# Kernel optimization log

Hardware: AMD Instinct MI355X
Metric: run time of the kernel (lower is better)

The kernel has to match this reference:

```python
import jax, jax.numpy as jnp
import numpy as np

B, H, T, D = 2, 8, 2048, 64
STATE = H * D  # 512

def setup_inputs() -> dict:
    key = jax.random.key(0)
    kq, kk, kv, kw, kl = jax.random.split(key, 5)
    q = jax.random.normal(kq, (B * H, T, D), jnp.float32)
    k = jax.random.normal(kk, (B * H, T, D), jnp.float32)
    v = jax.random.normal(kv, (B * H, T, D), jnp.float32)
    # causal position mask: True = masked (future positions)
    position_mask = jnp.triu(jnp.ones((T, T), dtype=bool), 1)
    # per-batch source lengths in [T//2, T]; True = padding (masked)
    lengths = jax.random.randint(kl, (B,), T // 2, T + 1)
    src_length_mask = jnp.arange(T)[None, :] >= lengths[:, None]
    W_merge = jax.random.normal(kw, (STATE, STATE), jnp.float32) / np.sqrt(STATE)
    return {"q": q, "k": k, "v": v, "position_mask": position_mask,
            "src_length_mask": src_length_mask, "W_merge": W_merge}

def reference(q, k, v, position_mask, src_length_mask, W_merge):
    bb, n_dest, d = q.shape              # bb = B*H
    n_batch = src_length_mask.shape[0]
    n_heads = bb // n_batch
    scale = 1.0 / np.sqrt(d)
    # [bb, T_dest, T_src] full score matrix (as in the torch bmm)
    logits = jnp.einsum('btd,bsd->bts', q, k) * scale
    logits = logits.reshape(n_batch, n_heads, n_dest, -1)
    logits = jnp.where(position_mask[None, None], -jnp.inf, logits)
    logits = jnp.where(src_length_mask[:, None, None, :], -jnp.inf, logits)
    scores = jax.nn.softmax(logits, axis=-1).reshape(bb, n_dest, -1)
    # dropout p=0 (eval) -> identity
    out = jnp.einsum('bts,bsd->btd', scores, v)
    out = out.reshape(n_batch, n_heads, n_dest, d).transpose(0, 2, 1, 3)
    out = out.reshape(n_batch, n_dest, n_heads * d)
    return out @ W_merge.T  # bias-free Linear merge
```

## Files before the change

kernel.cpp:

```cpp
#include <hip/hip_runtime.h>

#define TT 2048
#define DD 64
#define NSTATE 512

typedef __attribute__((ext_vector_type(8))) short short8;
typedef __attribute__((ext_vector_type(4))) short short4v;
typedef __attribute__((ext_vector_type(4))) float f4;

union U8 { short8 s; unsigned u[4]; };
union U4 { short4v s; unsigned u[2]; };

__device__ __forceinline__ unsigned pk_bf16(float lo, float hi) {
  unsigned r;
  asm("v_cvt_pk_bf16_f32 %0, %1, %2" : "=v"(r) : "v"(lo), "v"(hi));
  return r;
}
__device__ __forceinline__ unsigned short f2bf1(float x) {
  return (unsigned short)(pk_bf16(x, x) & 0xFFFFu);
}

__device__ __forceinline__ bool mask_at(const void* p, bool u8, int idx) {
  return u8 ? (((const unsigned char*)p)[idx] != 0)
            : (((const int*)p)[idx] != 0);
}

__device__ __forceinline__ void gld16(const void* g, void* l) {
  __builtin_amdgcn_global_load_lds(
      (const __attribute__((address_space(1))) void*)g,
      (__attribute__((address_space(3))) void*)l, 16, 0, 0);
}

__global__ __launch_bounds__(256)
void prep_kernel(const float* __restrict__ k, const float* __restrict__ v,
                 const float* __restrict__ W, const void* __restrict__ posmask,
                 const void* __restrict__ srcmask,
                 unsigned short* __restrict__ Wb, unsigned short* __restrict__ Kimg,
                 unsigned short* __restrict__ VTimg, int* __restrict__ lenbuf) {
  const int bidx = blockIdx.x;
  const int tid = threadIdx.x;
  if (bidx < 512) {
    const int bh = bidx >> 5, tile = bidx & 31;
    const float* kp = k + (bh * TT + tile * 64) * DD;
    unsigned short* dst = Kimg + (bh * 32 + tile) * 4096;
#pragma unroll
    for (int t2 = 0; t2 < 2; ++t2) {
      int j = tid + t2 * 256;
      int c8 = j >> 6, r6 = j & 63;
      int kb = c8 >> 1, cc = c8 & 1, qd = r6 >> 4, klo = r6 & 15;
      int key = kb * 16 + klo, dg = cc * 4 + qd;
      f4 a0 = *(const f4*)(kp + key * DD + dg * 8);
      f4 a1 = *(const f4*)(kp + key * DD + dg * 8 + 4);
      U8 o;
      o.u[0] = pk_bf16(a0[0], a0[1]); o.u[1] = pk_bf16(a0[2], a0[3]);
      o.u[2] = pk_bf16(a1[0], a1[1]); o.u[3] = pk_bf16(a1[2], a1[3]);
      *(short8*)(dst + j * 8) = o.s;
    }
    __shared__ float Vt[64][65];
    const float* vp = v + (bh * TT + tile * 64) * DD;
    {
      int key = tid >> 2, c0 = (tid & 3) * 16;
#pragma unroll
      for (int i = 0; i < 4; ++i) {
        f4 x = *(const f4*)(vp + key * DD + c0 + i * 4);
        Vt[key][c0 + i * 4 + 0] = x[0];
        Vt[key][c0 + i * 4 + 1] = x[1];
        Vt[key][c0 + i * 4 + 2] = x[2];
        Vt[key][c0 + i * 4 + 3] = x[3];
      }
    }
    __syncthreads();
    unsigned short* vd = VTimg + (bh * 32 + tile) * 4096;
#pragma unroll
    for (int t2 = 0; t2 < 2; ++t2) {
      int j = tid + t2 * 256;
      int fs = j >> 5;
      int db = fs >> 2, sb = fs & 3;
      int jj = j & 31;
      float t[8];
#pragma unroll
      for (int ii = 0; ii < 8; ++ii) {
        int l = jj * 2 + (ii >> 2), r = ii & 3;
        int s = sb * 16 + (l >> 4) * 4 + r;
        int d = db * 16 + (l & 15);
        t[ii] = Vt[s][d];
      }
      U8 o;
      o.u[0] = pk_bf16(t[0], t[1]); o.u[1] = pk_bf16(t[2], t[3]);
      o.u[2] = pk_bf16(t[4], t[5]); o.u[3] = pk_bf16(t[6], t[7]);
      *(short8*)(vd + j * 8) = o.s;
    }
  } else if (bidx < 768) {
    int i = ((bidx - 512) * 256 + tid) * 4;
    f4 x = *(const f4*)(W + i);
    U4 o;
    o.u[0] = pk_bf16(x[0], x[1]); o.u[1] = pk_bf16(x[2], x[3]);
    *(short4v*)(Wb + i) = o.s;
  } else {
    const int wv = tid >> 6, lane = tid & 63;
    if (wv < 2) {
      const bool u8 = (((const unsigned char*)posmask)[1] != 0);
      int pos = 1024 + lane * 16;
      bool m1 = mask_at(srcmask, u8, wv * TT + pos);
      unsigned long long bal = __ballot(m1);
      int cur = bal ? (1024 + (__ffsll((unsigned long long)bal) - 1) * 16) : 2048;
      int prev = cur - 16;
      bool m2 = false;
      if (lane < 16) {
        int pos2 = prev + 1 + lane;
        m2 = (pos2 < TT) ? mask_at(srcmask, u8, wv * TT + pos2) : true;
      }
      unsigned long long bal2 = __ballot(m2);
      int len = prev + 1 + (__ffsll((unsigned long long)bal2) - 1);
      if (lane == 0) lenbuf[wv] = len;
    }
  }
}

__global__ __launch_bounds__(512, 4)
void attn_kernel(const float* __restrict__ q, const unsigned short* __restrict__ Kimg,
                 const unsigned short* __restrict__ VTimg,
                 const int* __restrict__ lenbuf, unsigned short* __restrict__ merged) {
  const int i = blockIdx.x;
  const int bh = ((i & 7) << 1) | ((i >> 3) & 1);
  const int tr = i >> 4;
  const int tile = (tr < 16) ? tr : 47 - tr;
  const int b = bh >> 3, h = bh & 7;
  const int tid = threadIdx.x;
  const int w = tid >> 6, lane = tid & 63;
  const int g = w >> 2, wl = w & 3;
  const int lane_lo = lane & 15, quad = lane >> 4;
  const int q0 = tile * 64 + wl * 16;
  const int len = lenbuf[b];
  const int n_st = min(tile + 1, (len + 63) >> 6);
  const int trips = (n_st + 1) >> 1;

  __shared__ __attribute__((aligned(16))) unsigned short Klds[2][2][4096];
  __shared__ __attribute__((aligned(16))) unsigned short Vlds[2][2][4096];

  short8 qf[2];
  {
    const float* qrow = q + ((bh * TT) + q0 + lane_lo) * DD;
#pragma unroll
    for (int c = 0; c < 2; ++c) {
      int d0 = c * 32 + quad * 8;
      f4 a0 = *(const f4*)(qrow + d0);
      f4 a1 = *(const f4*)(qrow + d0 + 4);
      U8 t;
      t.u[0] = pk_bf16(a0[0] * 0.125f, a0[1] * 0.125f);
      t.u[1] = pk_bf16(a0[2] * 0.125f, a0[3] * 0.125f);
      t.u[2] = pk_bf16(a1[0] * 0.125f, a1[1] * 0.125f);
      t.u[3] = pk_bf16(a1[2] * 0.125f, a1[3] * 0.125f);
      qf[c] = t.s;
    }
  }
  asm volatile("s_waitcnt vmcnt(0)" ::: "memory");

  float l_lane = 0.f;
  f4 O[4];
#pragma unroll
  for (int d = 0; d < 4; ++d) O[d] = (f4){0.f, 0.f, 0.f, 0.f};

  const char* kbase = (const char*)Kimg + (size_t)bh * 262144;
  const char* vbase = (const char*)VTimg + (size_t)bh * 262144;

  auto stage = [&](int st, int bufi) {
    const char* ks = kbase + st * 8192 + wl * 2048 + lane * 16;
    char* kl = (char*)&Klds[g][bufi][0] + wl * 2048 + lane * 16;
    gld16(ks, kl); gld16(ks + 1024, kl + 1024);
    const char* vs = vbase + st * 8192 + wl * 2048 + lane * 16;
    char* vl = (char*)&Vlds[g][bufi][0] + wl * 2048 + lane * 16;
    gld16(vs, vl); gld16(vs + 1024, vl + 1024);
  };

  if (g < n_st) stage(g, 0);

  for (int it = 0; it < trips; ++it) {
    const int st = 2 * it + g;
    const int bufc = it & 1;
    if (st + 2 < n_st) {
      stage(st + 2, bufc ^ 1);
      asm volatile("s_waitcnt vmcnt(4)" ::: "memory");
    } else {
      asm volatile("s_waitcnt vmcnt(0)" ::: "memory");
    }
    __builtin_amdgcn_s_barrier();
    __builtin_amdgcn_sched_barrier(0);

    if (st < n_st) {
      const unsigned short* Kl = &Klds[g][bufc][0];
      const unsigned short* Vl = &Vlds[g][bufc][0];
      const int s0 = st * 64;

      f4 ST[4];
      __builtin_amdgcn_s_setprio(1);
#pragma unroll
      for (int sb = 0; sb < 4; ++sb) {
        f4 acc = (f4){0.f, 0.f, 0.f, 0.f};
#pragma unroll
        for (int c = 0; c < 2; ++c) {
          short8 kf = *(const short8*)&Kl[((sb * 2 + c) * 64 + lane) * 8];
          acc = __builtin_amdgcn_mfma_f32_16x16x32_bf16(kf, qf[c], acc, 0, 0, 0);
        }
        ST[sb] = acc;
      }
      __builtin_amdgcn_s_setprio(0);

      const bool edge = (st == tile) || (s0 + 64 > len);
      const int tq = q0 + lane_lo;
      short4v pf[4];
#pragma unroll
      for (int sb = 0; sb < 4; ++sb) {
        float e[4];
#pragma unroll
        for (int r = 0; r < 4; ++r) {
          float p = __expf(ST[sb][r]);
          if (edge) {
            int s = s0 + sb * 16 + quad * 4 + r;
            if (s > tq || s >= len) p = 0.f;
          }
          l_lane += p;
          e[r] = p;
        }
        U4 pu;
        pu.u[0] = pk_bf16(e[0], e[1]);
        pu.u[1] = pk_bf16(e[2], e[3]);
        pf[sb] = pu.s;
      }

      __builtin_amdgcn_s_setprio(1);
#pragma unroll
      for (int db = 0; db < 4; ++db) {
        f4 acc = O[db];
#pragma unroll
        for (int sb = 0; sb < 4; ++sb) {
          short4v vf = *(const short4v*)&Vl[(db * 4 + sb) * 256 + lane * 4];
          acc = __builtin_amdgcn_mfma_f32_16x16x16bf16_1k(pf[sb], vf, acc, 0, 0, 0);
        }
        O[db] = acc;
      }
      __builtin_amdgcn_s_setprio(0);
    }
    __builtin_amdgcn_sched_barrier(0);
    __builtin_amdgcn_s_barrier();
  }

  l_lane += __shfl_xor(l_lane, 16);
  l_lane += __shfl_xor(l_lane, 32);

  float* Ored = (float*)&Klds[1][0][0];
  float* lred = (float*)&Vlds[1][0][0];
  if (g == 1) {
    float* po = Ored + (wl * 64 + lane) * 16;
#pragma unroll
    for (int db = 0; db < 4; ++db) *(f4*)(po + db * 4) = O[db];
    lred[wl * 64 + lane] = l_lane;
  }
  __syncthreads();
  if (g == 0) {
    const float* po = Ored + (wl * 64 + lane) * 16;
#pragma unroll
    for (int db = 0; db < 4; ++db) {
      f4 o1 = *(const f4*)(po + db * 4);
      O[db][0] += o1[0]; O[db][1] += o1[1];
      O[db][2] += o1[2]; O[db][3] += o1[3];
    }
    l_lane += lred[wl * 64 + lane];
    float inv = 1.0f / l_lane;
    float invr[4];
#pragma unroll
    for (int r = 0; r < 4; ++r) invr[r] = __shfl(inv, quad * 4 + r);
#pragma unroll
    for (int db = 0; db < 4; ++db)
#pragma unroll
      for (int r = 0; r < 4; ++r) {
        int t = q0 + quad * 4 + r;
        merged[((b * TT) + t) * NSTATE + h * DD + db * 16 + lane_lo] =
            f2bf1(O[db][r] * invr[r]);
      }
  }
}

__global__ __launch_bounds__(512)
void merge_kernel(const unsigned short* __restrict__ A,
                  const unsigned short* __restrict__ Wb,
                  float* __restrict__ out) {
  __shared__ __attribute__((aligned(16))) unsigned short Wl[64 * 512];
  const int tid = threadIdx.x;
  const int n0 = blockIdx.x * 64, m0 = blockIdx.y * 128;
  {
    int row = tid >> 3, cb = (tid & 7) * 8;
    const unsigned short* src = Wb + (n0 + row) * NSTATE;
#pragma unroll
    for (int j = 0; j < 8; ++j) {
      int c = cb + j;
      int phys = c ^ (row & 7);
      *(short8*)&Wl[row * 512 + phys * 8] = *(const short8*)(src + c * 8);
    }
  }
  __syncthreads();

  const int w = tid >> 6, lane = tid & 63;
  const int lo16 = lane & 15, quad = lane >> 4;
  const int m = m0 + w * 16;
  f4 acc[4];
#pragma unroll
  for (int nf = 0; nf < 4; ++nf) acc[nf] = (f4){0.f, 0.f, 0.f, 0.f};
  const unsigned short* arow = A + (m + lo16) * NSTATE + quad * 8;
#pragma unroll 4
  for (int k0 = 0; k0 < NSTATE; k0 += 32) {
    short8 af = *(const short8*)(arow + k0);
#pragma unroll
    for (int nf = 0; nf < 4; ++nf) {
      int n = nf * 16 + lo16;
      int phys = ((k0 >> 3) + quad) ^ (n & 7);
      short8 bf = *(const short8*)&Wl[n * 512 + phys * 8];
      acc[nf] = __builtin_amdgcn_mfma_f32_16x16x32_bf16(af, bf, acc[nf], 0, 0, 0);
    }
  }
#pragma unroll
  for (int nf = 0; nf < 4; ++nf)
#pragma unroll
    for (int r = 0; r < 4; ++r)
      out[(m + quad * 4 + r) * NSTATE + n0 + nf * 16 + lo16] = acc[nf][r];
}

extern "C" void kernel_launch(void* const* d_in, const int* in_sizes, int n_in,
                              void* d_out, int out_size, void* d_ws, size_t ws_size,
                              hipStream_t stream) {
  (void)in_sizes; (void)n_in; (void)out_size; (void)ws_size;
  const float* q = (const float*)d_in[0];
  const float* k = (const float*)d_in[1];
  const float* v = (const float*)d_in[2];
  const void* posm = d_in[3];
  const void* srcm = d_in[4];
  const float* W = (const float*)d_in[5];
  float* out = (float*)d_out;

  unsigned short* merged = (unsigned short*)d_ws;
  unsigned short* Wb     = merged + 2097152;
  unsigned short* Kimg   = Wb + 262144;
  unsigned short* VTimg  = Kimg + 2097152;
  int* lenbuf = (int*)(VTimg + 2097152);

  prep_kernel<<<dim3(769), dim3(256), 0, stream>>>(k, v, W, posm, srcm,
                                                   Wb, Kimg, VTimg, lenbuf);
  attn_kernel<<<dim3(512), dim3(512), 0, stream>>>(q, Kimg, VTimg, lenbuf, merged);
  merge_kernel<<<dim3(8, 32), dim3(512), 0, stream>>>(merged, Wb, out);
}
```

Before: 121.1 us.

## Split attention keys four ways with 32-row query tiles per warp

Each warp now handles 32 query rows, up from 16, so every K and V fragment read from LDS feeds two MFMAs. The key dimension is split into 32-key sub-tiles across four warp groups instead of 64-key tiles across two, and the V image layout is rearranged so one 16-byte load supplies both halves. Sub-tiles that lie entirely above a warp's causal diagonal are skipped. In exchange the cross-group reduction of O and l through shared memory grows from one partner group to three, and register pressure rises.

```diff
diff --git a/kernel.cpp b/kernel.cpp
--- a/kernel.cpp
+++ b/kernel.cpp
@@ -18,6 +18,13 @@
 }
 __device__ __forceinline__ unsigned short f2bf1(float x) {
   return (unsigned short)(pk_bf16(x, x) & 0xFFFFu);
+}
+
+__device__ __forceinline__ short4v lo4(short8 x) {
+  short4v r; r[0] = x[0]; r[1] = x[1]; r[2] = x[2]; r[3] = x[3]; return r;
+}
+__device__ __forceinline__ short4v hi4(short8 x) {
+  short4v r; r[0] = x[4]; r[1] = x[5]; r[2] = x[6]; r[3] = x[7]; return r;
 }
 
 __device__ __forceinline__ bool mask_at(const void* p, bool u8, int idx) {
@@ -74,14 +81,14 @@
 #pragma unroll
     for (int t2 = 0; t2 < 2; ++t2) {
       int j = tid + t2 * 256;
-      int fs = j >> 5;
-      int db = fs >> 2, sb = fs & 3;
-      int jj = j & 31;
+      int hd = j >> 6;
+      int hh = hd >> 2, db = hd & 3;
+      int l = j & 63;
       float t[8];
 #pragma unroll
       for (int ii = 0; ii < 8; ++ii) {
-        int l = jj * 2 + (ii >> 2), r = ii & 3;
-        int s = sb * 16 + (l >> 4) * 4 + r;
+        int sbl = ii >> 2, r = ii & 3;
+        int s = hh * 32 + sbl * 16 + (l >> 4) * 4 + r;
         int d = db * 16 + (l & 15);
         t[ii] = Vt[s][d];
       }
@@ -128,19 +135,19 @@
   const int b = bh >> 3, h = bh & 7;
   const int tid = threadIdx.x;
   const int w = tid >> 6, lane = tid & 63;
-  const int g = w >> 2, wl = w & 3;
+  const int g = w >> 1, wl = w & 1;
   const int lane_lo = lane & 15, quad = lane >> 4;
-  const int q0 = tile * 64 + wl * 16;
+  const int q0 = tile * 64 + wl * 32;
   const int len = lenbuf[b];
-  const int n_st = min(tile + 1, (len + 63) >> 6);
-  const int trips = (n_st + 1) >> 1;
-
-  __shared__ __attribute__((aligned(16))) unsigned short Klds[2][2][4096];
-  __shared__ __attribute__((aligned(16))) unsigned short Vlds[2][2][4096];
-
-  short8 qf[2];
-  {
-    const float* qrow = q + ((bh * TT) + q0 + lane_lo) * DD;
+  const int n_ss = min(2 * (tile + 1), (len + 31) >> 5);
+  const int trips = (n_ss + 3) >> 2;
+
+  __shared__ __attribute__((aligned(16))) unsigned char smem[65536];
+
+  short8 qf[2][2];
+#pragma unroll
+  for (int qb = 0; qb < 2; ++qb) {
+    const float* qrow = q + ((bh * TT) + q0 + qb * 16 + lane_lo) * DD;
 #pragma unroll
     for (int c = 0; c < 2; ++c) {
       int d0 = c * 32 + quad * 8;
@@ -151,35 +158,38 @@
       t.u[1] = pk_bf16(a0[2] * 0.125f, a0[3] * 0.125f);
       t.u[2] = pk_bf16(a1[0] * 0.125f, a1[1] * 0.125f);
       t.u[3] = pk_bf16(a1[2] * 0.125f, a1[3] * 0.125f);
-      qf[c] = t.s;
+      qf[qb][c] = t.s;
     }
   }
   asm volatile("s_waitcnt vmcnt(0)" ::: "memory");
 
-  float l_lane = 0.f;
-  f4 O[4];
-#pragma unroll
-  for (int d = 0; d < 4; ++d) O[d] = (f4){0.f, 0.f, 0.f, 0.f};
+  float l_lane[2] = {0.f, 0.f};
+  f4 O[2][4];
+#pragma unroll
+  for (int qb = 0; qb < 2; ++qb)
+#pragma unroll
+    for (int d = 0; d < 4; ++d) O[qb][d] = (f4){0.f, 0.f, 0.f, 0.f};
 
   const char* kbase = (const char*)Kimg + (size_t)bh * 262144;
   const char* vbase = (const char*)VTimg + (size_t)bh * 262144;
 
-  auto stage = [&](int st, int bufi) {
-    const char* ks = kbase + st * 8192 + wl * 2048 + lane * 16;
-    char* kl = (char*)&Klds[g][bufi][0] + wl * 2048 + lane * 16;
-    gld16(ks, kl); gld16(ks + 1024, kl + 1024);
-    const char* vs = vbase + st * 8192 + wl * 2048 + lane * 16;
-    char* vl = (char*)&Vlds[g][bufi][0] + wl * 2048 + lane * 16;
-    gld16(vs, vl); gld16(vs + 1024, vl + 1024);
+  auto stage = [&](int ss, int bufi) {
+    const int gl = wl * 64 + lane;
+    const char* ks = kbase + ss * 4096 + gl * 16;
+    char* kl = (char*)smem + (g * 2 + bufi) * 4096 + gl * 16;
+    gld16(ks, kl); gld16(ks + 2048, kl + 2048);
+    const char* vs = vbase + ss * 4096 + gl * 16;
+    char* vl = (char*)smem + 32768 + (g * 2 + bufi) * 4096 + gl * 16;
+    gld16(vs, vl); gld16(vs + 2048, vl + 2048);
   };
 
-  if (g < n_st) stage(g, 0);
+  if (g < n_ss) stage(g, 0);
 
   for (int it = 0; it < trips; ++it) {
-    const int st = 2 * it + g;
+    const int ss = 4 * it + g;
     const int bufc = it & 1;
-    if (st + 2 < n_st) {
-      stage(st + 2, bufc ^ 1);
+    if (ss + 4 < n_ss) {
+      stage(ss + 4, bufc ^ 1);
       asm volatile("s_waitcnt vmcnt(4)" ::: "memory");
     } else {
       asm volatile("s_waitcnt vmcnt(0)" ::: "memory");
@@ -187,57 +197,61 @@
     __builtin_amdgcn_s_barrier();
     __builtin_amdgcn_sched_barrier(0);
 
-    if (st < n_st) {
-      const unsigned short* Kl = &Klds[g][bufc][0];
-      const unsigned short* Vl = &Vlds[g][bufc][0];
-      const int s0 = st * 64;
-
-      f4 ST[4];
+    const int s0 = ss * 32;
+    if (ss < n_ss && s0 <= q0 + 31) {
+      const unsigned short* Kl = (const unsigned short*)smem + (g * 2 + bufc) * 2048;
+      const unsigned short* Vl = (const unsigned short*)smem + 16384 + (g * 2 + bufc) * 2048;
+
+      f4 ST[2][2];
       __builtin_amdgcn_s_setprio(1);
 #pragma unroll
-      for (int sb = 0; sb < 4; ++sb) {
-        f4 acc = (f4){0.f, 0.f, 0.f, 0.f};
+      for (int sbl = 0; sbl < 2; ++sbl) {
+        f4 a0 = (f4){0.f, 0.f, 0.f, 0.f};
+        f4 a1 = (f4){0.f, 0.f, 0.f, 0.f};
 #pragma unroll
         for (int c = 0; c < 2; ++c) {
-          short8 kf = *(const short8*)&Kl[((sb * 2 + c) * 64 + lane) * 8];
-          acc = __builtin_amdgcn_mfma_f32_16x16x32_bf16(kf, qf[c], acc, 0, 0, 0);
+          short8 kf = *(const short8*)&Kl[((sbl * 2 + c) * 64 + lane) * 8];
+          a0 = __builtin_amdgcn_mfma_f32_16x16x32_bf16(kf, qf[0][c], a0, 0, 0, 0);
+          a1 = __builtin_amdgcn_mfma_f32_16x16x32_bf16(kf, qf[1][c], a1, 0, 0, 0);
         }
-        ST[sb] = acc;
+        ST[0][sbl] = a0; ST[1][sbl] = a1;
       }
       __builtin_amdgcn_s_setprio(0);
 
-      const bool edge = (st == tile) || (s0 + 64 > len);
-      const int tq = q0 + lane_lo;
-      short4v pf[4];
-#pragma unroll
-      for (int sb = 0; sb < 4; ++sb) {
-        float e[4];
-#pragma unroll
-        for (int r = 0; r < 4; ++r) {
-          float p = __expf(ST[sb][r]);
-          if (edge) {
-            int s = s0 + sb * 16 + quad * 4 + r;
-            if (s > tq || s >= len) p = 0.f;
+      const bool edge = (ss >= 2 * tile) || (s0 + 32 > len);
+      short4v pf[2][2];
+#pragma unroll
+      for (int qb = 0; qb < 2; ++qb) {
+        const int tq = q0 + qb * 16 + lane_lo;
+#pragma unroll
+        for (int sbl = 0; sbl < 2; ++sbl) {
+          float e[4];
+#pragma unroll
+          for (int r = 0; r < 4; ++r) {
+            float p = __expf(ST[qb][sbl][r]);
+            if (edge) {
+              int s = s0 + sbl * 16 + quad * 4 + r;
+              if (s > tq || s >= len) p = 0.f;
+            }
+            l_lane[qb] += p;
+            e[r] = p;
           }
-          l_lane += p;
-          e[r] = p;
+          U4 pu;
+          pu.u[0] = pk_bf16(e[0], e[1]);
+          pu.u[1] = pk_bf16(e[2], e[3]);
+          pf[qb][sbl] = pu.s;
         }
-        U4 pu;
-        pu.u[0] = pk_bf16(e[0], e[1]);
-        pu.u[1] = pk_bf16(e[2], e[3]);
-        pf[sb] = pu.s;
       }
 
       __builtin_amdgcn_s_setprio(1);
 #pragma unroll
       for (int db = 0; db < 4; ++db) {
-        f4 acc = O[db];
-#pragma unroll
-        for (int sb = 0; sb < 4; ++sb) {
-          short4v vf = *(const short4v*)&Vl[(db * 4 + sb) * 256 + lane * 4];
-          acc = __builtin_amdgcn_mfma_f32_16x16x16bf16_1k(pf[sb], vf, acc, 0, 0, 0);
-        }
-        O[db] = acc;
+        short8 vv = *(const short8*)&Vl[(db * 64 + lane) * 8];
+        short4v v0 = lo4(vv), v1 = hi4(vv);
+        O[0][db] = __builtin_amdgcn_mfma_f32_16x16x16bf16_1k(pf[0][0], v0, O[0][db], 0, 0, 0);
+        O[0][db] = __builtin_amdgcn_mfma_f32_16x16x16bf16_1k(pf[0][1], v1, O[0][db], 0, 0, 0);
+        O[1][db] = __builtin_amdgcn_mfma_f32_16x16x16bf16_1k(pf[1][0], v0, O[1][db], 0, 0, 0);
+        O[1][db] = __builtin_amdgcn_mfma_f32_16x16x16bf16_1k(pf[1][1], v1, O[1][db], 0, 0, 0);
       }
       __builtin_amdgcn_s_setprio(0);
     }
@@ -245,39 +259,57 @@
     __builtin_amdgcn_s_barrier();
   }
 
-  l_lane += __shfl_xor(l_lane, 16);
-  l_lane += __shfl_xor(l_lane, 32);
-
-  float* Ored = (float*)&Klds[1][0][0];
-  float* lred = (float*)&Vlds[1][0][0];
-  if (g == 1) {
-    float* po = Ored + (wl * 64 + lane) * 16;
-#pragma unroll
-    for (int db = 0; db < 4; ++db) *(f4*)(po + db * 4) = O[db];
-    lred[wl * 64 + lane] = l_lane;
+#pragma unroll
+  for (int qb = 0; qb < 2; ++qb) {
+    l_lane[qb] += __shfl_xor(l_lane[qb], 16);
+    l_lane[qb] += __shfl_xor(l_lane[qb], 32);
+  }
+
+  float* Opub = (float*)smem;
+  float* lpub = (float*)(smem + 49152);
+  if (g > 0) {
+    const int slot = (g - 1) * 2 + wl;
+    float* po = Opub + slot * 2048 + lane * 32;
+#pragma unroll
+    for (int qb = 0; qb < 2; ++qb)
+#pragma unroll
+      for (int db = 0; db < 4; ++db)
+        *(f4*)(po + qb * 16 + db * 4) = O[qb][db];
+    lpub[slot * 128 + lane * 2 + 0] = l_lane[0];
+    lpub[slot * 128 + lane * 2 + 1] = l_lane[1];
   }
   __syncthreads();
   if (g == 0) {
-    const float* po = Ored + (wl * 64 + lane) * 16;
-#pragma unroll
-    for (int db = 0; db < 4; ++db) {
-      f4 o1 = *(const f4*)(po + db * 4);
-      O[db][0] += o1[0]; O[db][1] += o1[1];
-      O[db][2] += o1[2]; O[db][3] += o1[3];
-    }
-    l_lane += lred[wl * 64 + lane];
-    float inv = 1.0f / l_lane;
-    float invr[4];
-#pragma unroll
-    for (int r = 0; r < 4; ++r) invr[r] = __shfl(inv, quad * 4 + r);
-#pragma unroll
-    for (int db = 0; db < 4; ++db)
-#pragma unroll
-      for (int r = 0; r < 4; ++r) {
-        int t = q0 + quad * 4 + r;
-        merged[((b * TT) + t) * NSTATE + h * DD + db * 16 + lane_lo] =
-            f2bf1(O[db][r] * invr[r]);
-      }
+#pragma unroll
+    for (int sl = 0; sl < 3; ++sl) {
+      const int slot = sl * 2 + wl;
+      const float* po = Opub + slot * 2048 + lane * 32;
+#pragma unroll
+      for (int qb = 0; qb < 2; ++qb)
+#pragma unroll
+        for (int db = 0; db < 4; ++db) {
+          f4 o1 = *(const f4*)(po + qb * 16 + db * 4);
+          O[qb][db][0] += o1[0]; O[qb][db][1] += o1[1];
+          O[qb][db][2] += o1[2]; O[qb][db][3] += o1[3];
+        }
+      l_lane[0] += lpub[slot * 128 + lane * 2 + 0];
+      l_lane[1] += lpub[slot * 128 + lane * 2 + 1];
+    }
+#pragma unroll
+    for (int qb = 0; qb < 2; ++qb) {
+      float inv = 1.0f / l_lane[qb];
+      float invr[4];
+#pragma unroll
+      for (int r = 0; r < 4; ++r) invr[r] = __shfl(inv, quad * 4 + r);
+#pragma unroll
+      for (int db = 0; db < 4; ++db)
+#pragma unroll
+        for (int r = 0; r < 4; ++r) {
+          int t = q0 + qb * 16 + quad * 4 + r;
+          merged[((b * TT) + t) * NSTATE + h * DD + db * 16 + lane_lo] =
+              f2bf1(O[qb][db][r] * invr[r]);
+        }
+    }
   }
 }
 
```

New measurement: 123.3 us. Within noise of the previous version (+1.9%).

## Fuse merge projection into attention epilogue with atomic accumulation per head

Applied to the files above, without the earlier changes.

Removes the separate merge GEMM kernel and the bf16 intermediate buffer. Each attention block now stages its normalized 64x64 output tile in LDS, multiplies it by that head's 64-column slice of W_merge, and atomically adds the partial 64x512 products into the fp32 output. The prep kernel zeroes the output first. This saves one launch and a global round-trip of the merged activations, but adds eight-way float atomic traffic per output element, extra epilogue work in each attention block, and a summation order that is no longer deterministic.

```diff
diff --git a/kernel.cpp b/kernel.cpp
--- a/kernel.cpp
+++ b/kernel.cpp
@@ -36,9 +36,15 @@
                  const float* __restrict__ W, const void* __restrict__ posmask,
                  const void* __restrict__ srcmask,
                  unsigned short* __restrict__ Wb, unsigned short* __restrict__ Kimg,
-                 unsigned short* __restrict__ VTimg, int* __restrict__ lenbuf) {
+                 unsigned short* __restrict__ VTimg, int* __restrict__ lenbuf,
+                 float* __restrict__ out) {
   const int bidx = blockIdx.x;
   const int tid = threadIdx.x;
+  {
+    const f4 z = (f4){0.f, 0.f, 0.f, 0.f};
+    for (int j = bidx * 256 + tid; j < 524288; j += 769 * 256)
+      *(f4*)(out + j * 4) = z;
+  }
   if (bidx < 512) {
     const int bh = bidx >> 5, tile = bidx & 31;
     const float* kp = k + (bh * TT + tile * 64) * DD;
@@ -120,7 +126,8 @@
 __global__ __launch_bounds__(512, 4)
 void attn_kernel(const float* __restrict__ q, const unsigned short* __restrict__ Kimg,
                  const unsigned short* __restrict__ VTimg,
-                 const int* __restrict__ lenbuf, unsigned short* __restrict__ merged) {
+                 const int* __restrict__ lenbuf, const unsigned short* __restrict__ Wb,
+                 float* __restrict__ out) {
   const int i = blockIdx.x;
   const int bh = ((i & 7) << 1) | ((i >> 3) & 1);
   const int tr = i >> 4;
@@ -135,8 +142,7 @@
   const int n_st = min(tile + 1, (len + 63) >> 6);
   const int trips = (n_st + 1) >> 1;
 
-  __shared__ __attribute__((aligned(16))) unsigned short Klds[2][2][4096];
-  __shared__ __attribute__((aligned(16))) unsigned short Vlds[2][2][4096];
+  __shared__ __attribute__((aligned(16))) unsigned short smem[32768];
 
   short8 qf[2];
   {
@@ -166,10 +172,10 @@
 
   auto stage = [&](int st, int bufi) {
     const char* ks = kbase + st * 8192 + wl * 2048 + lane * 16;
-    char* kl = (char*)&Klds[g][bufi][0] + wl * 2048 + lane * 16;
+    char* kl = (char*)smem + (g * 2 + bufi) * 8192 + wl * 2048 + lane * 16;
     gld16(ks, kl); gld16(ks + 1024, kl + 1024);
     const char* vs = vbase + st * 8192 + wl * 2048 + lane * 16;
-    char* vl = (char*)&Vlds[g][bufi][0] + wl * 2048 + lane * 16;
+    char* vl = (char*)smem + 32768 + (g * 2 + bufi) * 8192 + wl * 2048 + lane * 16;
     gld16(vs, vl); gld16(vs + 1024, vl + 1024);
   };
 
@@ -188,8 +194,8 @@
     __builtin_amdgcn_sched_barrier(0);
 
     if (st < n_st) {
-      const unsigned short* Kl = &Klds[g][bufc][0];
-      const unsigned short* Vl = &Vlds[g][bufc][0];
+      const unsigned short* Kl = smem + (g * 2 + bufc) * 4096;
+      const unsigned short* Vl = smem + 16384 + (g * 2 + bufc) * 4096;
       const int s0 = st * 64;
 
       f4 ST[4];
@@ -248,8 +254,8 @@
   l_lane += __shfl_xor(l_lane, 16);
   l_lane += __shfl_xor(l_lane, 32);
 
-  float* Ored = (float*)&Klds[1][0][0];
-  float* lred = (float*)&Vlds[1][0][0];
+  float* Ored = (float*)((char*)smem + 16384);
+  float* lred = (float*)((char*)smem + 49152);
   if (g == 1) {
     float* po = Ored + (wl * 64 + lane) * 16;
 #pragma unroll
@@ -257,6 +263,8 @@
     lred[wl * 64 + lane] = l_lane;
   }
   __syncthreads();
+
+  unsigned short* Am = smem;
   if (g == 0) {
     const float* po = Ored + (wl * 64 + lane) * 16;
 #pragma unroll
@@ -274,55 +282,60 @@
     for (int db = 0; db < 4; ++db)
 #pragma unroll
       for (int r = 0; r < 4; ++r) {
-        int t = q0 + quad * 4 + r;
-        merged[((b * TT) + t) * NSTATE + h * DD + db * 16 + lane_lo] =
+        int m = wl * 16 + quad * 4 + r;
+        int d = db * 16 + lane_lo;
+        Am[m * 64 + (((d >> 3) ^ (m & 7)) * 8) + (d & 7)] =
             f2bf1(O[db][r] * invr[r]);
       }
   }
-}
-
-__global__ __launch_bounds__(512)
-void merge_kernel(const unsigned short* __restrict__ A,
-                  const unsigned short* __restrict__ Wb,
-                  float* __restrict__ out) {
-  __shared__ __attribute__((aligned(16))) unsigned short Wl[64 * 512];
-  const int tid = threadIdx.x;
-  const int n0 = blockIdx.x * 64, m0 = blockIdx.y * 128;
-  {
-    int row = tid >> 3, cb = (tid & 7) * 8;
-    const unsigned short* src = Wb + (n0 + row) * NSTATE;
-#pragma unroll
-    for (int j = 0; j < 8; ++j) {
-      int c = cb + j;
-      int phys = c ^ (row & 7);
-      *(short8*)&Wl[row * 512 + phys * 8] = *(const short8*)(src + c * 8);
-    }
-  }
   __syncthreads();
 
-  const int w = tid >> 6, lane = tid & 63;
-  const int lo16 = lane & 15, quad = lane >> 4;
-  const int m = m0 + w * 16;
-  f4 acc[4];
-#pragma unroll
-  for (int nf = 0; nf < 4; ++nf) acc[nf] = (f4){0.f, 0.f, 0.f, 0.f};
-  const unsigned short* arow = A + (m + lo16) * NSTATE + quad * 8;
-#pragma unroll 4
-  for (int k0 = 0; k0 < NSTATE; k0 += 32) {
-    short8 af = *(const short8*)(arow + k0);
-#pragma unroll
-    for (int nf = 0; nf < 4; ++nf) {
-      int n = nf * 16 + lo16;
-      int phys = ((k0 >> 3) + quad) ^ (n & 7);
-      short8 bf = *(const short8*)&Wl[n * 512 + phys * 8];
-      acc[nf] = __builtin_amdgcn_mfma_f32_16x16x32_bf16(af, bf, acc[nf], 0, 0, 0);
-    }
-  }
-#pragma unroll
-  for (int nf = 0; nf < 4; ++nf)
-#pragma unroll
-    for (int r = 0; r < 4; ++r)
-      out[(m + quad * 4 + r) * NSTATE + n0 + nf * 16 + lo16] = acc[nf][r];
+  short8 af[4][2];
+#pragma unroll
+  for (int mb = 0; mb < 4; ++mb)
+#pragma unroll
+    for (int c = 0; c < 2; ++c)
+      af[mb][c] = *(const short8*)&Am[(mb * 16 + lane_lo) * 64 +
+                                      (((c * 4 + quad) ^ (lane_lo & 7)) * 8)];
+  unsigned short* Wl = smem + 4096;
+  const unsigned short* wsrc = Wb + h * 64;
+  const int n0w = w * 32;
+#pragma unroll
+  for (int nh = 0; nh < 2; ++nh) {
+    {
+      int n = tid >> 1, cb = (tid & 1) * 4;
+      const unsigned short* src = wsrc + (nh * 256 + n) * NSTATE;
+#pragma unroll
+      for (int jj = 0; jj < 4; ++jj) {
+        int c8 = cb + jj;
+        *(short8*)&Wl[n * 64 + ((c8 ^ (n & 7)) * 8)] = *(const short8*)(src + c8 * 8);
+      }
+    }
+    __syncthreads();
+    short8 bfw[2][2];
+#pragma unroll
+    for (int nf = 0; nf < 2; ++nf)
+#pragma unroll
+      for (int c = 0; c < 2; ++c) {
+        int n = n0w + nf * 16 + lane_lo;
+        bfw[nf][c] = *(const short8*)&Wl[n * 64 + (((c * 4 + quad) ^ (n & 7)) * 8)];
+      }
+#pragma unroll
+    for (int mb = 0; mb < 4; ++mb)
+#pragma unroll
+      for (int nf = 0; nf < 2; ++nf) {
+        f4 acc = (f4){0.f, 0.f, 0.f, 0.f};
+        acc = __builtin_amdgcn_mfma_f32_16x16x32_bf16(af[mb][0], bfw[nf][0], acc, 0, 0, 0);
+        acc = __builtin_amdgcn_mfma_f32_16x16x32_bf16(af[mb][1], bfw[nf][1], acc, 0, 0, 0);
+#pragma unroll
+        for (int rr = 0; rr < 4; ++rr) {
+          int t = tile * 64 + mb * 16 + quad * 4 + rr;
+          atomicAdd(&out[((b * TT) + t) * NSTATE + nh * 256 + n0w + nf * 16 + lane_lo],
+                    acc[rr]);
+        }
+      }
+    if (nh == 0) __syncthreads();
+  }
 }
 
 extern "C" void kernel_launch(void* const* d_in, const int* in_sizes, int n_in,
@@ -337,14 +350,12 @@
   const float* W = (const float*)d_in[5];
   float* out = (float*)d_out;
 
-  unsigned short* merged = (unsigned short*)d_ws;
-  unsigned short* Wb     = merged + 2097152;
-  unsigned short* Kimg   = Wb + 262144;
-  unsigned short* VTimg  = Kimg + 2097152;
+  unsigned short* Wb   = (unsigned short*)d_ws;
+  unsigned short* Kimg = Wb + 262144;
+  unsigned short* VTimg = Kimg + 2097152;
   int* lenbuf = (int*)(VTimg + 2097152);
 
   prep_kernel<<<dim3(769), dim3(256), 0, stream>>>(k, v, W, posm, srcm,
-                                                   Wb, Kimg, VTimg, lenbuf);
-  attn_kernel<<<dim3(512), dim3(512), 0, stream>>>(q, Kimg, VTimg, lenbuf, merged);
-  merge_kernel<<<dim3(8, 32), dim3(512), 0, stream>>>(merged, Wb, out);
-}
+                                                   Wb, Kimg, VTimg, lenbuf, out);
+  attn_kernel<<<dim3(512), dim3(512), 0, stream>>>(q, Kimg, VTimg, lenbuf, Wb, out);
+}
```

Result: slower. 147.2 us (+21.5%).

## Halve attention tile to 32 queries and keys with 1024 smaller blocks

Applied to the files above, without the earlier changes.

The attention kernel now uses 256-thread blocks that each handle 32 query rows, stepping over 32-key sub-tiles. It launches 1024 blocks instead of 512, and the V image layout is reordered so one 16-byte LDS read feeds two MFMAs. The goal is better load balance across CUs for the causal triangle and less wasted work on diagonal and edge tiles, since the masking granularity becomes 32. The cost is more blocks, more barriers per key processed, and Q being reloaded more often relative to K/V traffic.

```diff
diff --git a/kernel.cpp b/kernel.cpp
--- a/kernel.cpp
+++ b/kernel.cpp
@@ -18,6 +18,13 @@
 }
 __device__ __forceinline__ unsigned short f2bf1(float x) {
   return (unsigned short)(pk_bf16(x, x) & 0xFFFFu);
+}
+
+__device__ __forceinline__ short4v lo4(short8 x) {
+  short4v r; r[0] = x[0]; r[1] = x[1]; r[2] = x[2]; r[3] = x[3]; return r;
+}
+__device__ __forceinline__ short4v hi4(short8 x) {
+  short4v r; r[0] = x[4]; r[1] = x[5]; r[2] = x[6]; r[3] = x[7]; return r;
 }
 
 __device__ __forceinline__ bool mask_at(const void* p, bool u8, int idx) {
@@ -74,14 +81,14 @@
 #pragma unroll
     for (int t2 = 0; t2 < 2; ++t2) {
       int j = tid + t2 * 256;
-      int fs = j >> 5;
-      int db = fs >> 2, sb = fs & 3;
-      int jj = j & 31;
+      int hd = j >> 6;
+      int hh = hd >> 2, db = hd & 3;
+      int l = j & 63;
       float t[8];
 #pragma unroll
       for (int ii = 0; ii < 8; ++ii) {
-        int l = jj * 2 + (ii >> 2), r = ii & 3;
-        int s = sb * 16 + (l >> 4) * 4 + r;
+        int sbl = ii >> 2, r = ii & 3;
+        int s = hh * 32 + sbl * 16 + (l >> 4) * 4 + r;
         int d = db * 16 + (l & 15);
         t[ii] = Vt[s][d];
       }
@@ -117,26 +124,25 @@
   }
 }
 
-__global__ __launch_bounds__(512, 4)
+__global__ __launch_bounds__(256, 4)
 void attn_kernel(const float* __restrict__ q, const unsigned short* __restrict__ Kimg,
                  const unsigned short* __restrict__ VTimg,
                  const int* __restrict__ lenbuf, unsigned short* __restrict__ merged) {
   const int i = blockIdx.x;
   const int bh = ((i & 7) << 1) | ((i >> 3) & 1);
-  const int tr = i >> 4;
-  const int tile = (tr < 16) ? tr : 47 - tr;
+  const int qtr = i >> 4;
+  const int qt = (qtr & 1) ? 63 - (qtr >> 1) : (qtr >> 1);
   const int b = bh >> 3, h = bh & 7;
   const int tid = threadIdx.x;
   const int w = tid >> 6, lane = tid & 63;
-  const int g = w >> 2, wl = w & 3;
+  const int g = w >> 1, wl = w & 1;
   const int lane_lo = lane & 15, quad = lane >> 4;
-  const int q0 = tile * 64 + wl * 16;
+  const int q0 = qt * 32 + wl * 16;
   const int len = lenbuf[b];
-  const int n_st = min(tile + 1, (len + 63) >> 6);
-  const int trips = (n_st + 1) >> 1;
-
-  __shared__ __attribute__((aligned(16))) unsigned short Klds[2][2][4096];
-  __shared__ __attribute__((aligned(16))) unsigned short Vlds[2][2][4096];
+  const int n_ss = min(qt + 1, (len + 31) >> 5);
+  const int trips = (n_ss + 1) >> 1;
+
+  __shared__ __attribute__((aligned(16))) unsigned short smem[16384];
 
   short8 qf[2];
   {
@@ -164,22 +170,23 @@
   const char* kbase = (const char*)Kimg + (size_t)bh * 262144;
   const char* vbase = (const char*)VTimg + (size_t)bh * 262144;
 
-  auto stage = [&](int st, int bufi) {
-    const char* ks = kbase + st * 8192 + wl * 2048 + lane * 16;
-    char* kl = (char*)&Klds[g][bufi][0] + wl * 2048 + lane * 16;
-    gld16(ks, kl); gld16(ks + 1024, kl + 1024);
-    const char* vs = vbase + st * 8192 + wl * 2048 + lane * 16;
-    char* vl = (char*)&Vlds[g][bufi][0] + wl * 2048 + lane * 16;
-    gld16(vs, vl); gld16(vs + 1024, vl + 1024);
+  auto stage = [&](int ss, int bufi) {
+    const int gl = wl * 64 + lane;
+    const char* ks = kbase + ss * 4096 + gl * 16;
+    char* kl = (char*)smem + (g * 2 + bufi) * 4096 + gl * 16;
+    gld16(ks, kl); gld16(ks + 2048, kl + 2048);
+    const char* vs = vbase + ss * 4096 + gl * 16;
+    char* vl = (char*)smem + 16384 + (g * 2 + bufi) * 4096 + gl * 16;
+    gld16(vs, vl); gld16(vs + 2048, vl + 2048);
   };
 
-  if (g < n_st) stage(g, 0);
+  if (g < n_ss) stage(g, 0);
 
   for (int it = 0; it < trips; ++it) {
-    const int st = 2 * it + g;
+    const int ss = 2 * it + g;
     const int bufc = it & 1;
-    if (st + 2 < n_st) {
-      stage(st + 2, bufc ^ 1);
+    if (ss + 2 < n_ss) {
+      stage(ss + 2, bufc ^ 1);
       asm volatile("s_waitcnt vmcnt(4)" ::: "memory");
     } else {
       asm volatile("s_waitcnt vmcnt(0)" ::: "memory");
@@ -187,36 +194,36 @@
     __builtin_amdgcn_s_barrier();
     __builtin_amdgcn_sched_barrier(0);
 
-    if (st < n_st) {
-      const unsigned short* Kl = &Klds[g][bufc][0];
-      const unsigned short* Vl = &Vlds[g][bufc][0];
-      const int s0 = st * 64;
-
-      f4 ST[4];
+    if (ss < n_ss) {
+      const unsigned short* Kl = smem + (g * 2 + bufc) * 2048;
+      const unsigned short* Vl = smem + 8192 + (g * 2 + bufc) * 2048;
+      const int s0 = ss * 32;
+
+      f4 ST[2];
       __builtin_amdgcn_s_setprio(1);
 #pragma unroll
-      for (int sb = 0; sb < 4; ++sb) {
+      for (int sbl = 0; sbl < 2; ++sbl) {
         f4 acc = (f4){0.f, 0.f, 0.f, 0.f};
 #pragma unroll
         for (int c = 0; c < 2; ++c) {
-          short8 kf = *(const short8*)&Kl[((sb * 2 + c) * 64 + lane) * 8];
+          short8 kf = *(const short8*)&Kl[((sbl * 2 + c) * 64 + lane) * 8];
           acc = __builtin_amdgcn_mfma_f32_16x16x32_bf16(kf, qf[c], acc, 0, 0, 0);
         }
-        ST[sb] = acc;
+        ST[sbl] = acc;
       }
       __builtin_amdgcn_s_setprio(0);
 
-      const bool edge = (st == tile) || (s0 + 64 > len);
+      const bool edge = (ss == qt) || (s0 + 32 > len);
       const int tq = q0 + lane_lo;
-      short4v pf[4];
-#pragma unroll
-      for (int sb = 0; sb < 4; ++sb) {
+      short4v pf[2];
+#pragma unroll
+      for (int sbl = 0; sbl < 2; ++sbl) {
         float e[4];
 #pragma unroll
         for (int r = 0; r < 4; ++r) {
-          float p = __expf(ST[sb][r]);
+          float p = __expf(ST[sbl][r]);
           if (edge) {
-            int s = s0 + sb * 16 + quad * 4 + r;
+            int s = s0 + sbl * 16 + quad * 4 + r;
             if (s > tq || s >= len) p = 0.f;
           }
           l_lane += p;
@@ -225,18 +232,16 @@
         U4 pu;
         pu.u[0] = pk_bf16(e[0], e[1]);
         pu.u[1] = pk_bf16(e[2], e[3]);
-        pf[sb] = pu.s;
+        pf[sbl] = pu.s;
       }
 
       __builtin_amdgcn_s_setprio(1);
 #pragma unroll
       for (int db = 0; db < 4; ++db) {
+        short8 vv = *(const short8*)&Vl[(db * 64 + lane) * 8];
         f4 acc = O[db];
-#pragma unroll
-        for (int sb = 0; sb < 4; ++sb) {
-          short4v vf = *(const short4v*)&Vl[(db * 4 + sb) * 256 + lane * 4];
-          acc = __builtin_amdgcn_mfma_f32_16x16x16bf16_1k(pf[sb], vf, acc, 0, 0, 0);
-        }
+        acc = __builtin_amdgcn_mfma_f32_16x16x16bf16_1k(pf[0], lo4(vv), acc, 0, 0, 0);
+        acc = __builtin_amdgcn_mfma_f32_16x16x16bf16_1k(pf[1], hi4(vv), acc, 0, 0, 0);
         O[db] = acc;
       }
       __builtin_amdgcn_s_setprio(0);
@@ -248,8 +253,8 @@
   l_lane += __shfl_xor(l_lane, 16);
   l_lane += __shfl_xor(l_lane, 32);
 
-  float* Ored = (float*)&Klds[1][0][0];
-  float* lred = (float*)&Vlds[1][0][0];
+  float* Ored = (float*)((char*)smem + 8192);
+  float* lred = (float*)((char*)smem + 16384 + 8192);
   if (g == 1) {
     float* po = Ored + (wl * 64 + lane) * 16;
 #pragma unroll
@@ -345,6 +350,6 @@
 
   prep_kernel<<<dim3(769), dim3(256), 0, stream>>>(k, v, W, posm, srcm,
                                                    Wb, Kimg, VTimg, lenbuf);
-  attn_kernel<<<dim3(512), dim3(512), 0, stream>>>(q, Kimg, VTimg, lenbuf, merged);
+  attn_kernel<<<dim3(1024), dim3(256), 0, stream>>>(q, Kimg, VTimg, lenbuf, merged);
   merge_kernel<<<dim3(8, 32), dim3(512), 0, stream>>>(merged, Wb, out);
 }
```

Measured after the change: 121.2 us. Within noise of the previous version (+0.1%).
